# Optimization experiments

Hardware: AMD Instinct MI355X
Metric: run time of the kernel (lower is better)

## Reference

```python
import jax, jax.numpy as jnp
import numpy as np

NG, NPG = 16384, 8            # graphs, nodes per graph
N = NG * NPG                   # total nodes
EPS = 1e-5                     # BatchNorm eps
SLOPE = 0.01                   # leaky_relu negative slope
DIMS = [6, 16, 16, 32, 64, 128]


def _gcn(x, src, dst, w_e, W, b):
    # PyG GCNConv with edge weights and implicit self-loops (weight 1):
    # h = x W; out = D^-1/2 (A + I) D^-1/2 h + b, deg from dst incl. self-loop
    h = x @ W
    deg = jnp.zeros((N,), h.dtype).at[dst].add(w_e) + 1.0
    dis = jax.lax.rsqrt(deg)
    norm = dis[src] * w_e * dis[dst]                      # [E]
    out = jnp.zeros_like(h).at[dst].add(norm[:, None] * h[src])
    out = out + h * (dis * dis)[:, None]                  # self-loop term deg^-1 * h
    return out + b


def _bn(x, g, be):
    # training-mode BatchNorm1d over nodes (biased variance)
    m = x.mean(0)
    v = ((x - m) ** 2).mean(0)
    return g * (x - m) * jax.lax.rsqrt(v + EPS) + be


def _lrelu(x):
    return jnp.where(x >= 0, x, SLOPE * x)


def setup_inputs() -> dict:
    key = jax.random.key(0)
    ks = jax.random.split(key, 16)
    # fully-connected directed edges within each 8-node graph (no self-loops)
    s, d = np.meshgrid(np.arange(NPG), np.arange(NPG), indexing='ij')
    m = s != d
    s, d = s[m], d[m]                                     # 56 per graph
    offs = (np.arange(NG) * NPG)[:, None]
    src = (offs + s[None, :]).ravel()
    dst = (offs + d[None, :]).ravel()
    E = src.size
    inp = {
        'x': jax.random.normal(ks[0], (N, DIMS[0]), jnp.float32),
        'edge_index': jnp.asarray(np.stack([src, dst]), dtype=jnp.int32),
        'edge_attr': jax.random.uniform(ks[1], (E,), jnp.float32),
        'batch': jnp.asarray(np.repeat(np.arange(NG), NPG), dtype=jnp.int32),
    }
    for i in range(5):
        inp[f'w{i+1}'] = jax.random.normal(ks[2 + i], (DIMS[i], DIMS[i + 1]), jnp.float32) * (1.0 / np.sqrt(DIMS[i]).astype(np.float32))
        inp[f'b{i+1}'] = jnp.zeros((DIMS[i + 1],), jnp.float32)
        inp[f'g{i+1}'] = jnp.ones((DIMS[i + 1],), jnp.float32)
        inp[f'be{i+1}'] = jnp.zeros((DIMS[i + 1],), jnp.float32)
    inp['fc1_w'] = jax.random.normal(ks[7], (128, 30), jnp.float32) * 0.1
    inp['fc1_b'] = jnp.zeros((30,), jnp.float32)
    inp['fc2_w'] = jax.random.normal(ks[8], (30, 20), jnp.float32) * 0.1
    inp['fc2_b'] = jnp.zeros((20,), jnp.float32)
    inp['out_w'] = jax.random.normal(ks[9], (20, 1), jnp.float32) * 0.1
    inp['out_b'] = jnp.zeros((1,), jnp.float32)
    return inp


def reference(x, edge_index, edge_attr, batch,
              w1, b1, g1, be1, w2, b2, g2, be2, w3, b3, g3, be3,
              w4, b4, g4, be4, w5, b5, g5, be5,
              fc1_w, fc1_b, fc2_w, fc2_b, out_w, out_b):
    src, dst = edge_index[0], edge_index[1]
    layers = [(w1, b1, g1, be1), (w2, b2, g2, be2), (w3, b3, g3, be3),
              (w4, b4, g4, be4), (w5, b5, g5, be5)]
    h = x
    for (W, b, g, be) in layers:
        h = _lrelu(_bn(_gcn(h, src, dst, edge_attr, W, b), g, be))
    # global mean pool: each graph has exactly NPG nodes
    pooled = jax.ops.segment_sum(h, batch, num_segments=NG) / NPG
    z = _lrelu(pooled @ fc1_w + fc1_b)
    z = _lrelu(z @ fc2_w + fc2_b)      # dropout is identity in eval mode
    return z @ out_w + out_b           # [NG, 1]
```

## Files before the change

kernel.cpp:

```cpp
#include <hip/hip_runtime.h>

#define NN 131072
#define NBLK 256
#define THREADS 512
#define NODES_B 512
#define GRAPHS_B 64
constexpr float BN_EPS = 1e-5f;
constexpr float NSLOPE = 0.01f;

typedef unsigned short ushortT;
typedef short v8s __attribute__((ext_vector_type(8)));
typedef float v4f __attribute__((ext_vector_type(4)));

__device__ __forceinline__ float lrelu(float x) { return x >= 0.0f ? x : NSLOPE * x; }
__device__ __forceinline__ ushortT f2bf(float f) {
    unsigned int u = __float_as_uint(f);
    u += 0x7fffu + ((u >> 16) & 1u);
    return (ushortT)(u >> 16);
}

__global__ void zero_ws_kernel(float* __restrict__ p) { p[threadIdx.x] = 0.0f; }

struct Params {
    const float *x, *ea;
    const float *w1,*b1,*g1,*be1, *w2,*b2,*g2,*be2, *w3,*b3,*g3,*be3;
    const float *w4,*b4,*g4,*be4, *w5,*b5,*g5,*be5;
    const float *fc1w,*fc1b,*fc2w,*fc2b,*ow,*ob;
    float* stats;
    unsigned int* bar;
    float* outp;
};

__device__ __forceinline__ void gbar(unsigned int* bar, int tid) {
    __syncthreads();
    if (tid == 0) {
        __hip_atomic_fetch_add(bar, 1u, __ATOMIC_RELEASE, __HIP_MEMORY_SCOPE_AGENT);
        int guard = 0;
        while (__hip_atomic_load(bar, __ATOMIC_RELAXED, __HIP_MEMORY_SCOPE_AGENT) < (unsigned)NBLK
               && guard < (1 << 24)) { __builtin_amdgcn_s_sleep(1); ++guard; }
    }
    __syncthreads();
}

template<int DIN>
__device__ __forceinline__ void agg_shfl(const float* xr, float* Y, const float* coef,
                                         int lane, int d) {
    #pragma unroll
    for (int k = 0; k < DIN; k++) Y[k] = coef[0] * xr[k];
    #pragma unroll
    for (int r = 1; r < 8; r++) {
        int srcLane = (lane & ~7) | ((d + r) & 7);
        float cr = coef[r];
        #pragma unroll
        for (int k = 0; k < DIN; k++)
            Y[k] = fmaf(cr, __shfl(xr[k], srcLane), Y[k]);
    }
}

template<int DIN, int DOUT>
__device__ __forceinline__ void gemm_lane(const float* Y, const float* Wl,
                                          const float* bias, float* acc) {
    #pragma unroll
    for (int j = 0; j < DOUT; j++) acc[j] = bias[j];
    #pragma unroll
    for (int k = 0; k < DIN; k++) {
        float yk = Y[k];
        #pragma unroll
        for (int j = 0; j < DOUT; j++)
            acc[j] = fmaf(yk, Wl[k * DOUT + j], acc[j]);
    }
}

template<int DOUT>
__device__ __forceinline__ void stats_from_hbuf(const float* hbuf, float* red,
                                                float* statsL, int tid) {
    __syncthreads();
    constexpr int SEG = THREADS / DOUT;
    int c = tid % DOUT, seg = tid / DOUT;
    float s = 0.f, q = 0.f;
    #pragma unroll 4
    for (int i = 0; i < DOUT; i++) {
        float v = hbuf[(seg * DOUT + i) * 33 + c];
        s += v; q = fmaf(v, v, q);
    }
    red[seg * 2 * DOUT + c] = s;
    red[seg * 2 * DOUT + DOUT + c] = q;
    __syncthreads();
    if (tid < 2 * DOUT) {
        float t = 0.f;
        #pragma unroll
        for (int sg = 0; sg < SEG; sg++) t += red[sg * 2 * DOUT + tid];
        atomicAdd(&statsL[tid], t);
    }
}

template<int DIN>
__device__ __forceinline__ void bn_params(const float* statsL, const float* g,
                                          const float* be, float* scS, float* shS, int tid) {
    if (tid < DIN) {
        float s = __hip_atomic_load(&statsL[tid], __ATOMIC_RELAXED, __HIP_MEMORY_SCOPE_AGENT);
        float q = __hip_atomic_load(&statsL[DIN + tid], __ATOMIC_RELAXED, __HIP_MEMORY_SCOPE_AGENT);
        float mean = s * (1.0f / NN);
        float var = fmaf(-mean, mean, q * (1.0f / NN));
        float scl = g[tid] * rsqrtf(var + BN_EPS);
        scS[tid] = scl;
        shS[tid] = fmaf(-mean, scl, be[tid]);
    }
    __syncthreads();
}

__device__ __forceinline__ v8s ld_v8(const ushortT* p) {
    union { v8s v; uint2 u[2]; } t;
    t.u[0] = *(const uint2*)p;
    t.u[1] = *(const uint2*)(p + 4);
    return t.v;
}

#define SMEM_TOTAL 153472

__global__ __launch_bounds__(THREADS, 2) void fused_kernel(Params P)
{
    __shared__ __align__(16) char smem[SMEM_TOTAL];
    float*   hbuf   = (float*)smem;
    ushortT* Y4b    = (ushortT*)smem;
    ushortT* X5T    = (ushortT*)smem;
    float*   pooled = (float*)smem;
    float*   WesS   = (float*)(smem + 67584);
    float*   disS   = (float*)(smem + 81920);
    float*   AcS    = (float*)(smem + 83968);
    ushortT* X4T    = (ushortT*)(smem + 67584);
    ushortT* Y5b    = (ushortT*)(smem + 67584);
    float*   z1s    = (float*)(smem + 67584);
    float*   z2s    = (float*)(smem + 75776);
    float*   W123   = (float*)(smem + 137216);
    ushortT* W4t    = (ushortT*)(smem + 140672);
    float*   red    = (float*)(smem + 145280);
    float*   scS    = red;
    float*   shS    = red + 128;

    const int tid  = threadIdx.x;
    const int lane = tid & 63;
    const int w    = tid >> 6;
    const int m16  = lane & 15;
    const int quad = lane >> 4;
    const int d    = tid & 7;
    const int gloc = tid >> 3;

    const int g0 = blockIdx.x * GRAPHS_B;
    for (int e = tid; e < GRAPHS_B * 56; e += THREADS) WesS[e] = P.ea[(size_t)g0 * 56 + e];
    if (tid < 96)  W123[tid] = P.w1[tid];
    if (tid < 256) W123[96 + tid] = P.w2[tid];
    W123[352 + tid] = P.w3[tid];
    for (int e = tid; e < 2048; e += THREADS) {
        int c = e >> 5, k = e & 31;
        W4t[c * 36 + k] = f2bf(P.w4[(size_t)k * 64 + c]);
    }
    __syncthreads();

    {
        float deg = 1.0f;
        #pragma unroll
        for (int s = 0; s < 8; s++)
            if (s != d) deg += WesS[gloc * 56 + s * 7 + (d > s ? d - 1 : d)];
        disS[tid] = rsqrtf(deg);
    }
    __syncthreads();

    float coef[8];
    {
        float dis = disS[tid];
        coef[0] = dis * dis;
        #pragma unroll
        for (int r = 1; r < 8; r++) {
            int s = (d + r) & 7;
            float we = WesS[gloc * 56 + s * 7 + (d > s ? d - 1 : d)];
            coef[r] = dis * we * disS[(tid & ~7) | s];
        }
    }
    for (int e = tid; e < GRAPHS_B * 64; e += THREADS) {
        int g = e >> 6, s = (e >> 3) & 7, dd = e & 7;
        float v;
        if (s == dd) { float t = disS[g * 8 + dd]; v = t * t; }
        else v = disS[g * 8 + s] * WesS[g * 56 + s * 7 + (dd > s ? dd - 1 : dd)] * disS[g * 8 + dd];
        AcS[g * 68 + s * 8 + dd] = v;
    }
    __syncthreads();

    v8s AcM[4];
    #pragma unroll
    for (int Gl = 0; Gl < 4; Gl++) {
        int G = 4 * w + Gl;
        int koct = 2 * (G & 1) + (m16 >> 3);
        int gA = 2 * G + (m16 >> 3);
        ushortT tmp[8];
        #pragma unroll
        for (int j = 0; j < 8; j++)
            tmp[j] = (quad == koct) ? f2bf(AcS[gA * 68 + j * 8 + (m16 & 7)]) : (ushortT)0;
        AcM[Gl] = *(v8s*)tmp;
    }
    v8s W5f[8][2];
    #pragma unroll
    for (int ct = 0; ct < 8; ct++)
        #pragma unroll
        for (int kh = 0; kh < 2; kh++) {
            ushortT tmp[8];
            #pragma unroll
            for (int j = 0; j < 8; j++)
                tmp[j] = f2bf(P.w5[(size_t)(kh * 32 + quad * 8 + j) * 128 + ct * 16 + m16]);
            W5f[ct][kh] = *(v8s*)tmp;
        }

    const int gnode = blockIdx.x * NODES_B + tid;
    float xr[16];
    {
        const float2* px = (const float2*)(P.x + (size_t)gnode * 6);
        float2 a = px[0], b = px[1], c = px[2];
        xr[0]=a.x; xr[1]=a.y; xr[2]=b.x; xr[3]=b.y; xr[4]=c.x; xr[5]=c.y;
    }
    {
        float Y[6], acc[16];
        agg_shfl<6>(xr, Y, coef, lane, d);
        gemm_lane<6,16>(Y, W123, P.b1, acc);
        #pragma unroll
        for (int j = 0; j < 16; j++) hbuf[tid * 33 + j] = acc[j];
    }
    stats_from_hbuf<16>(hbuf, red, P.stats + 0, tid);
    gbar(P.bar + 0, tid);
    bn_params<16>(P.stats + 0, P.g1, P.be1, scS, shS, tid);

    {
        #pragma unroll
        for (int k = 0; k < 16; k++)
            xr[k] = lrelu(fmaf(scS[k], hbuf[tid * 33 + k], shS[k]));
        float Y[16], acc[16];
        agg_shfl<16>(xr, Y, coef, lane, d);
        gemm_lane<16,16>(Y, W123 + 96, P.b2, acc);
        #pragma unroll
        for (int j = 0; j < 16; j++) hbuf[tid * 33 + j] = acc[j];
    }
    stats_from_hbuf<16>(hbuf, red, P.stats + 32, tid);
    gbar(P.bar + 1, tid);
    bn_params<16>(P.stats + 32, P.g2, P.be2, scS, shS, tid);

    {
        #pragma unroll
        for (int k = 0; k < 16; k++)
            xr[k] = lrelu(fmaf(scS[k], hbuf[tid * 33 + k], shS[k]));
        float Y[16], acc[32];
        agg_shfl<16>(xr, Y, coef, lane, d);
        gemm_lane<16,32>(Y, W123 + 352, P.b3, acc);
        #pragma unroll
        for (int j = 0; j < 32; j++) hbuf[tid * 33 + j] = acc[j];
    }
    stats_from_hbuf<32>(hbuf, red, P.stats + 64, tid);
    gbar(P.bar + 2, tid);
    bn_params<32>(P.stats + 64, P.g3, P.be3, scS, shS, tid);

    #pragma unroll
    for (int it = 0; it < 8; it++) {
        int item = tid + it * THREADS;
        int c = item & 31, nq = item >> 5;
        float sc = scS[c], sh = shS[c];
        ushortT pk[4];
        #pragma unroll
        for (int i = 0; i < 4; i++)
            pk[i] = f2bf(lrelu(fmaf(sc, hbuf[(nq * 4 + i) * 33 + c], sh)));
        *(uint2*)&X4T[c * 520 + nq * 4] = *(uint2*)pk;
    }
    __syncthreads();

    {
        v8s Bf[2][2];
        #pragma unroll
        for (int Jl = 0; Jl < 2; Jl++) {
            int J = 2 * w + Jl;
            #pragma unroll
            for (int ct = 0; ct < 2; ct++)
                Bf[Jl][ct] = ld_v8(&X4T[(ct * 16 + m16) * 520 + 32 * J + quad * 8]);
        }
        #pragma unroll
        for (int Gl = 0; Gl < 4; Gl++) {
            int G = 4 * w + Gl;
            #pragma unroll
            for (int ct = 0; ct < 2; ct++) {
                v4f a = (v4f){0.f, 0.f, 0.f, 0.f};
                a = __builtin_amdgcn_mfma_f32_16x16x32_bf16(AcM[Gl], Bf[Gl >> 1][ct], a, 0, 0, 0);
                int ch = ct * 16 + m16;
                #pragma unroll
                for (int r = 0; r < 4; r++)
                    Y4b[(G * 16 + quad * 4 + r) * 36 + ch] = f2bf(a[r]);
            }
        }
    }
    __syncthreads();

    float b4r[4];
    #pragma unroll
    for (int ct = 0; ct < 4; ct++) b4r[ct] = P.b4[ct * 16 + m16];
    v4f acc4[4][4];
    {
        v8s W4fr[4];
        #pragma unroll
        for (int ct = 0; ct < 4; ct++)
            W4fr[ct] = ld_v8(&W4t[(ct * 16 + m16) * 36 + quad * 8]);
        #pragma unroll
        for (int rt = 0; rt < 4; rt++) {
            v8s Af = ld_v8(&Y4b[(w * 64 + rt * 16 + m16) * 36 + quad * 8]);
            #pragma unroll
            for (int ct = 0; ct < 4; ct++) {
                v4f a = (v4f){0.f, 0.f, 0.f, 0.f};
                a = __builtin_amdgcn_mfma_f32_16x16x32_bf16(Af, W4fr[ct], a, 0, 0, 0);
                #pragma unroll
                for (int r = 0; r < 4; r++) a[r] += b4r[ct];
                acc4[rt][ct] = a;
            }
        }
    }
    {
        float ps[4], pq[4];
        #pragma unroll
        for (int ct = 0; ct < 4; ct++) { ps[ct] = 0.f; pq[ct] = 0.f; }
        #pragma unroll
        for (int rt = 0; rt < 4; rt++)
            #pragma unroll
            for (int ct = 0; ct < 4; ct++)
                #pragma unroll
                for (int r = 0; r < 4; r++) {
                    float v = acc4[rt][ct][r];
                    ps[ct] += v; pq[ct] = fmaf(v, v, pq[ct]);
                }
        __syncthreads();
        #pragma unroll
        for (int ct = 0; ct < 4; ct++) {
            float s = ps[ct], q = pq[ct];
            s += __shfl_xor(s, 16); s += __shfl_xor(s, 32);
            q += __shfl_xor(q, 16); q += __shfl_xor(q, 32);
            if (lane < 16) {
                red[w * 256 + ct * 16 + lane] = s;
                red[w * 256 + 64 + ct * 16 + lane] = q;
            }
        }
        __syncthreads();
        if (tid < 128) {
            float t = 0.f;
            #pragma unroll
            for (int ww = 0; ww < 8; ww++) t += red[ww * 256 + tid];
            atomicAdd(&P.stats[128 + tid], t);
        }
    }
    gbar(P.bar + 3, tid);
    bn_params<64>(P.stats + 128, P.g4, P.be4, scS, shS, tid);

    #pragma unroll
    for (int rt = 0; rt < 4; rt++) {
        int nd0 = w * 64 + rt * 16 + quad * 4;
        #pragma unroll
        for (int ct = 0; ct < 4; ct++) {
            int c = ct * 16 + m16;
            float sc = scS[c], sh = shS[c];
            ushortT pk[4];
            #pragma unroll
            for (int r = 0; r < 4; r++)
                pk[r] = f2bf(lrelu(fmaf(sc, acc4[rt][ct][r], sh)));
            *(uint2*)&X5T[c * 520 + nd0] = *(uint2*)pk;
        }
    }
    __syncthreads();

    {
        v8s Bf[2][4];
        #pragma unroll
        for (int Jl = 0; Jl < 2; Jl++) {
            int J = 2 * w + Jl;
            #pragma unroll
            for (int ct = 0; ct < 4; ct++)
                Bf[Jl][ct] = ld_v8(&X5T[(ct * 16 + m16) * 520 + 32 * J + quad * 8]);
        }
        #pragma unroll
        for (int Gl = 0; Gl < 4; Gl++) {
            int G = 4 * w + Gl;
            #pragma unroll
            for (int ct = 0; ct < 4; ct++) {
                v4f a = (v4f){0.f, 0.f, 0.f, 0.f};
                a = __builtin_amdgcn_mfma_f32_16x16x32_bf16(AcM[Gl], Bf[Gl >> 1][ct], a, 0, 0, 0);
                int ch = ct * 16 + m16;
                #pragma unroll
                for (int r = 0; r < 4; r++)
                    Y5b[(G * 16 + quad * 4 + r) * 68 + ch] = f2bf(a[r]);
            }
        }
    }
    __syncthreads();

    float b5r[8];
    #pragma unroll
    for (int ct = 0; ct < 8; ct++) b5r[ct] = P.b5[ct * 16 + m16];
    v4f acc5[4][8];
    #pragma unroll
    for (int rt = 0; rt < 4; rt++) {
        v8s Af0 = ld_v8(&Y5b[(w * 64 + rt * 16 + m16) * 68 + quad * 8]);
        v8s Af1 = ld_v8(&Y5b[(w * 64 + rt * 16 + m16) * 68 + 32 + quad * 8]);
        #pragma unroll
        for (int ct = 0; ct < 8; ct++) {
            v4f a = (v4f){0.f, 0.f, 0.f, 0.f};
            a = __builtin_amdgcn_mfma_f32_16x16x32_bf16(Af0, W5f[ct][0], a, 0, 0, 0);
            a = __builtin_amdgcn_mfma_f32_16x16x32_bf16(Af1, W5f[ct][1], a, 0, 0, 0);
            #pragma unroll
            for (int r = 0; r < 4; r++) a[r] += b5r[ct];
            acc5[rt][ct] = a;
        }
    }
    {
        float ps[8], pq[8];
        #pragma unroll
        for (int ct = 0; ct < 8; ct++) { ps[ct] = 0.f; pq[ct] = 0.f; }
        #pragma unroll
        for (int rt = 0; rt < 4; rt++)
            #pragma unroll
            for (int ct = 0; ct < 8; ct++)
                #pragma unroll
                for (int r = 0; r < 4; r++) {
                    float v = acc5[rt][ct][r];
                    ps[ct] += v; pq[ct] = fmaf(v, v, pq[ct]);
                }
        __syncthreads();
        #pragma unroll
        for (int ct = 0; ct < 8; ct++) {
            float s = ps[ct], q = pq[ct];
            s += __shfl_xor(s, 16); s += __shfl_xor(s, 32);
            q += __shfl_xor(q, 16); q += __shfl_xor(q, 32);
            if (lane < 16) {
                red[w * 256 + ct * 16 + lane] = s;
                red[w * 256 + 128 + ct * 16 + lane] = q;
            }
        }
        __syncthreads();
        if (tid < 256) {
            float t = 0.f;
            #pragma unroll
            for (int ww = 0; ww < 8; ww++) t += red[ww * 256 + tid];
            atomicAdd(&P.stats[256 + tid], t);
        }
    }
    gbar(P.bar + 4, tid);
    bn_params<128>(P.stats + 256, P.g5, P.be5, scS, shS, tid);

    #pragma unroll
    for (int rt = 0; rt < 4; rt++) {
        int gA = 8 * w + 2 * rt + (quad >> 1);
        #pragma unroll
        for (int ct = 0; ct < 8; ct++) {
            int c = ct * 16 + m16;
            float sc = scS[c], sh = shS[c];
            float p = 0.f;
            #pragma unroll
            for (int r = 0; r < 4; r++)
                p += lrelu(fmaf(sc, acc5[rt][ct][r], sh));
            p += __shfl_xor(p, 16);
            if ((quad & 1) == 0) pooled[gA * 132 + c] = p * 0.125f;
        }
    }
    __syncthreads();

    const int t32 = tid & 31, gg = tid >> 5;
    for (int pass = 0; pass < 4; pass++) {
        int g = gg + pass * 16;
        if (t32 < 30) {
            float a = P.fc1b[t32];
            for (int k = 0; k < 128; k++) a = fmaf(pooled[g * 132 + k], P.fc1w[k * 30 + t32], a);
            z1s[g * 32 + t32] = lrelu(a);
        }
        __syncthreads();
        if (t32 < 20) {
            float a = P.fc2b[t32];
            #pragma unroll
            for (int k = 0; k < 30; k++) a = fmaf(z1s[g * 32 + k], P.fc2w[k * 20 + t32], a);
            z2s[g * 32 + t32] = lrelu(a);
        }
        __syncthreads();
        if (t32 == 0) {
            float a = P.ob[0];
            #pragma unroll
            for (int k = 0; k < 20; k++) a = fmaf(z2s[g * 32 + k], P.ow[k], a);
            P.outp[blockIdx.x * GRAPHS_B + g] = a;
        }
        __syncthreads();
    }
}

extern "C" void kernel_launch(void* const* d_in, const int* in_sizes, int n_in,
                              void* d_out, int out_size, void* d_ws, size_t ws_size,
                              hipStream_t stream)
{
    (void)in_sizes; (void)n_in; (void)out_size; (void)ws_size;
    float* stats = (float*)d_ws;

    Params hp;
    hp.x   = (const float*)d_in[0];
    hp.ea  = (const float*)d_in[2];
    hp.w1  = (const float*)d_in[4];  hp.b1  = (const float*)d_in[5];
    hp.g1  = (const float*)d_in[6];  hp.be1 = (const float*)d_in[7];
    hp.w2  = (const float*)d_in[8];  hp.b2  = (const float*)d_in[9];
    hp.g2  = (const float*)d_in[10]; hp.be2 = (const float*)d_in[11];
    hp.w3  = (const float*)d_in[12]; hp.b3  = (const float*)d_in[13];
    hp.g3  = (const float*)d_in[14]; hp.be3 = (const float*)d_in[15];
    hp.w4  = (const float*)d_in[16]; hp.b4  = (const float*)d_in[17];
    hp.g4  = (const float*)d_in[18]; hp.be4 = (const float*)d_in[19];
    hp.w5  = (const float*)d_in[20]; hp.b5  = (const float*)d_in[21];
    hp.g5  = (const float*)d_in[22]; hp.be5 = (const float*)d_in[23];
    hp.fc1w = (const float*)d_in[24]; hp.fc1b = (const float*)d_in[25];
    hp.fc2w = (const float*)d_in[26]; hp.fc2b = (const float*)d_in[27];
    hp.ow   = (const float*)d_in[28]; hp.ob   = (const float*)d_in[29];
    hp.stats = stats;
    hp.bar   = (unsigned int*)(stats + 512);
    hp.outp  = (float*)d_out;

    zero_ws_kernel<<<1, 1024, 0, stream>>>(stats);
    fused_kernel<<<NBLK, THREADS, 0, stream>>>(hp);
}
```

Baseline: 229.8 us.

## Replace grid barriers with counter-tagged fixed-point 64-bit stat atomics

Removes the five separate grid-wide barriers. Each batch-norm statistic is now a 64-bit fixed-point sum whose high bits count arriving blocks, and each stat gets its own 64-byte-spaced slot. Consumers spin on their own stat word until all blocks have contributed, so the barrier round-trip is dropped and the polling is spread over many addresses. In exchange the statistics use fixed-point quantization at 1/65536 resolution, which could lose precision on the sum of squares, and many threads now spin instead of one.

After: 228.2 us. No clear change (-0.7%).

```diff
diff --git a/kernel.cpp b/kernel.cpp
--- a/kernel.cpp
+++ b/kernel.cpp
@@ -9,6 +9,7 @@
 constexpr float NSLOPE = 0.01f;
 
 typedef unsigned short ushortT;
+typedef unsigned long long u64;
 typedef short v8s __attribute__((ext_vector_type(8)));
 typedef float v4f __attribute__((ext_vector_type(4)));
 
@@ -19,28 +20,27 @@
     return (ushortT)(u >> 16);
 }
 
-__global__ void zero_ws_kernel(float* __restrict__ p) { p[threadIdx.x] = 0.0f; }
+__device__ __forceinline__ u64 enc_stat(float t) {
+    long long v = (long long)llrintf(t * 65536.0f) + (1LL << 41);
+    return (1ULL << 52) + (u64)v;
+}
+__device__ __forceinline__ float dec_stat(u64 u) {
+    long long v = (long long)(u & ((1ULL << 52) - 1)) - ((long long)NBLK << 41);
+    return (float)((double)v * (1.0 / 65536.0));
+}
+
+__global__ void zero_ws_kernel(u64* __restrict__ p) {
+    for (int i = threadIdx.x; i < 4096; i += 1024) p[i] = 0ULL;
+}
 
 struct Params {
     const float *x, *ea;
     const float *w1,*b1,*g1,*be1, *w2,*b2,*g2,*be2, *w3,*b3,*g3,*be3;
     const float *w4,*b4,*g4,*be4, *w5,*b5,*g5,*be5;
     const float *fc1w,*fc1b,*fc2w,*fc2b,*ow,*ob;
-    float* stats;
-    unsigned int* bar;
+    u64* stats;
     float* outp;
 };
-
-__device__ __forceinline__ void gbar(unsigned int* bar, int tid) {
-    __syncthreads();
-    if (tid == 0) {
-        __hip_atomic_fetch_add(bar, 1u, __ATOMIC_RELEASE, __HIP_MEMORY_SCOPE_AGENT);
-        int guard = 0;
-        while (__hip_atomic_load(bar, __ATOMIC_RELAXED, __HIP_MEMORY_SCOPE_AGENT) < (unsigned)NBLK
-               && guard < (1 << 24)) { __builtin_amdgcn_s_sleep(1); ++guard; }
-    }
-    __syncthreads();
-}
 
 template<int DIN>
 __device__ __forceinline__ void agg_shfl(const float* xr, float* Y, const float* coef,
@@ -73,7 +73,7 @@
 
 template<int DOUT>
 __device__ __forceinline__ void stats_from_hbuf(const float* hbuf, float* red,
-                                                float* statsL, int tid) {
+                                                u64* statsL, int tid) {
     __syncthreads();
     constexpr int SEG = THREADS / DOUT;
     int c = tid % DOUT, seg = tid / DOUT;
@@ -90,16 +90,26 @@
         float t = 0.f;
         #pragma unroll
         for (int sg = 0; sg < SEG; sg++) t += red[sg * 2 * DOUT + tid];
-        atomicAdd(&statsL[tid], t);
+        __hip_atomic_fetch_add(&statsL[tid * 8], enc_stat(t),
+                               __ATOMIC_RELAXED, __HIP_MEMORY_SCOPE_AGENT);
     }
 }
 
 template<int DIN>
-__device__ __forceinline__ void bn_params(const float* statsL, const float* g,
+__device__ __forceinline__ void bn_params(const u64* statsL, const float* g,
                                           const float* be, float* scS, float* shS, int tid) {
+    __syncthreads();
     if (tid < DIN) {
-        float s = __hip_atomic_load(&statsL[tid], __ATOMIC_RELAXED, __HIP_MEMORY_SCOPE_AGENT);
-        float q = __hip_atomic_load(&statsL[DIN + tid], __ATOMIC_RELAXED, __HIP_MEMORY_SCOPE_AGENT);
+        u64 us, uq;
+        int guard = 0;
+        do {
+            us = __hip_atomic_load(&statsL[tid * 8], __ATOMIC_RELAXED, __HIP_MEMORY_SCOPE_AGENT);
+        } while ((us >> 52) < (u64)NBLK && ++guard < (1 << 26));
+        guard = 0;
+        do {
+            uq = __hip_atomic_load(&statsL[(DIN + tid) * 8], __ATOMIC_RELAXED, __HIP_MEMORY_SCOPE_AGENT);
+        } while ((uq >> 52) < (u64)NBLK && ++guard < (1 << 26));
+        float s = dec_stat(us), q = dec_stat(uq);
         float mean = s * (1.0f / NN);
         float var = fmaf(-mean, mean, q * (1.0f / NN));
         float scl = g[tid] * rsqrtf(var + BN_EPS);
@@ -139,6 +149,7 @@
     float*   shS    = red + 128;
 
     const int tid  = threadIdx.x;
+    const int bid  = blockIdx.x;
     const int lane = tid & 63;
     const int w    = tid >> 6;
     const int m16  = lane & 15;
@@ -146,7 +157,7 @@
     const int d    = tid & 7;
     const int gloc = tid >> 3;
 
-    const int g0 = blockIdx.x * GRAPHS_B;
+    const int g0 = bid * GRAPHS_B;
     for (int e = tid; e < GRAPHS_B * 56; e += THREADS) WesS[e] = P.ea[(size_t)g0 * 56 + e];
     if (tid < 96)  W123[tid] = P.w1[tid];
     if (tid < 256) W123[96 + tid] = P.w2[tid];
@@ -210,7 +221,7 @@
             W5f[ct][kh] = *(v8s*)tmp;
         }
 
-    const int gnode = blockIdx.x * NODES_B + tid;
+    const int gnode = bid * NODES_B + tid;
     float xr[16];
     {
         const float2* px = (const float2*)(P.x + (size_t)gnode * 6);
@@ -225,7 +236,6 @@
         for (int j = 0; j < 16; j++) hbuf[tid * 33 + j] = acc[j];
     }
     stats_from_hbuf<16>(hbuf, red, P.stats + 0, tid);
-    gbar(P.bar + 0, tid);
     bn_params<16>(P.stats + 0, P.g1, P.be1, scS, shS, tid);
 
     {
@@ -238,9 +248,8 @@
         #pragma unroll
         for (int j = 0; j < 16; j++) hbuf[tid * 33 + j] = acc[j];
     }
-    stats_from_hbuf<16>(hbuf, red, P.stats + 32, tid);
-    gbar(P.bar + 1, tid);
-    bn_params<16>(P.stats + 32, P.g2, P.be2, scS, shS, tid);
+    stats_from_hbuf<16>(hbuf, red, P.stats + 32 * 8, tid);
+    bn_params<16>(P.stats + 32 * 8, P.g2, P.be2, scS, shS, tid);
 
     {
         #pragma unroll
@@ -252,9 +261,8 @@
         #pragma unroll
         for (int j = 0; j < 32; j++) hbuf[tid * 33 + j] = acc[j];
     }
-    stats_from_hbuf<32>(hbuf, red, P.stats + 64, tid);
-    gbar(P.bar + 2, tid);
-    bn_params<32>(P.stats + 64, P.g3, P.be3, scS, shS, tid);
+    stats_from_hbuf<32>(hbuf, red, P.stats + 64 * 8, tid);
+    bn_params<32>(P.stats + 64 * 8, P.g3, P.be3, scS, shS, tid);
 
     #pragma unroll
     for (int it = 0; it < 8; it++) {
@@ -345,11 +353,11 @@
             float t = 0.f;
             #pragma unroll
             for (int ww = 0; ww < 8; ww++) t += red[ww * 256 + tid];
-            atomicAdd(&P.stats[128 + tid], t);
-        }
-    }
-    gbar(P.bar + 3, tid);
-    bn_params<64>(P.stats + 128, P.g4, P.be4, scS, shS, tid);
+            __hip_atomic_fetch_add(&P.stats[(128 + tid) * 8], enc_stat(t),
+                                   __ATOMIC_RELAXED, __HIP_MEMORY_SCOPE_AGENT);
+        }
+    }
+    bn_params<64>(P.stats + 128 * 8, P.g4, P.be4, scS, shS, tid);
 
     #pragma unroll
     for (int rt = 0; rt < 4; rt++) {
@@ -439,11 +447,11 @@
             float t = 0.f;
             #pragma unroll
             for (int ww = 0; ww < 8; ww++) t += red[ww * 256 + tid];
-            atomicAdd(&P.stats[256 + tid], t);
-        }
-    }
-    gbar(P.bar + 4, tid);
-    bn_params<128>(P.stats + 256, P.g5, P.be5, scS, shS, tid);
+            __hip_atomic_fetch_add(&P.stats[(256 + tid) * 8], enc_stat(t),
+                                   __ATOMIC_RELAXED, __HIP_MEMORY_SCOPE_AGENT);
+        }
+    }
+    bn_params<128>(P.stats + 256 * 8, P.g5, P.be5, scS, shS, tid);
 
     #pragma unroll
     for (int rt = 0; rt < 4; rt++) {
@@ -482,7 +490,7 @@
             float a = P.ob[0];
             #pragma unroll
             for (int k = 0; k < 20; k++) a = fmaf(z2s[g * 32 + k], P.ow[k], a);
-            P.outp[blockIdx.x * GRAPHS_B + g] = a;
+            P.outp[bid * GRAPHS_B + g] = a;
         }
         __syncthreads();
     }
@@ -493,7 +501,7 @@
                               hipStream_t stream)
 {
     (void)in_sizes; (void)n_in; (void)out_size; (void)ws_size;
-    float* stats = (float*)d_ws;
+    u64* stats = (u64*)d_ws;
 
     Params hp;
     hp.x   = (const float*)d_in[0];
@@ -512,7 +520,6 @@
     hp.fc2w = (const float*)d_in[26]; hp.fc2b = (const float*)d_in[27];
     hp.ow   = (const float*)d_in[28]; hp.ob   = (const float*)d_in[29];
     hp.stats = stats;
-    hp.bar   = (unsigned int*)(stats + 512);
     hp.outp  = (float*)d_out;
 
     zero_ws_kernel<<<1, 1024, 0, stream>>>(stats);
```
